# Performance work log

Measured on AMD Instinct MI355X. Metric: run time of the kernel, lower is better.

## Reference

```python
import jax, jax.numpy as jnp
import numpy as np

MAX_DEPTH = 6
NUM_TREES = 64
LEAF_DIMS = 128
D_IN = 512
BATCH = 4096
N_INTERNAL = 2 ** MAX_DEPTH - 1  # 63
N_LEAVES = 2 ** MAX_DEPTH        # 64


def setup_inputs() -> dict:
    key = jax.random.key(0)
    ks = jax.random.split(key, 4)
    x = jax.random.normal(ks[0], (BATCH, D_IN), dtype=jnp.float32)
    # Stacked internal-node dense layers, node i at index i (level order, node_index ordering)
    W = jax.random.normal(ks[1], (N_INTERNAL, D_IN, NUM_TREES), dtype=jnp.float32) / np.sqrt(D_IN)
    b = jnp.zeros((N_INTERNAL, NUM_TREES), dtype=jnp.float32)
    leaf_weight = jax.random.normal(ks[2], (N_LEAVES, LEAF_DIMS, NUM_TREES), dtype=jnp.float32)
    gates = jax.random.normal(ks[3], (N_LEAVES, LEAF_DIMS, NUM_TREES), dtype=jnp.float32)
    return {"x": x, "W": W, "b": b, "leaf_weight": leaf_weight, "gates": gates}


def reference(x, W, b, leaf_weight, gates):
    # All internal-node gating probabilities in one batched matmul:
    # g[b, n, t] = sigmoid(x[b] @ W[n] + b[n])  for every internal node n, tree t
    g = jax.nn.sigmoid(jnp.einsum('bd,ndt->bnt', x, W) + b[None, :, :])  # [B, 63, T]

    B = x.shape[0]
    T = W.shape[-1]
    # Path probability to each leaf, built level by level.
    # Level l has 2^l nodes at internal indices [2^l - 1, 2^(l+1) - 2];
    # interleaving (left=p*g, right=p*(1-g)) matches node_index child ordering.
    p = jnp.ones((B, 1, T), dtype=x.dtype)
    for level in range(MAX_DEPTH):
        start = 2 ** level - 1
        n_lvl = 2 ** level
        gl = g[:, start:start + n_lvl, :]                  # [B, n_lvl, T]
        children = jnp.stack([p * gl, p * (1.0 - gl)], axis=2)  # [B, n_lvl, 2, T]
        p = children.reshape(B, 2 * n_lvl, T)
    # p: [B, n_leaves, T] leaf path probabilities

    # Softmax mixture-of-experts gate over trees, then weighted leaf mixture:
    # out[b, d] = sum_{l, t} p[b, l, t] * leaf_weight[l, d, t] * softmax(gates, -1)[l, d, t]
    w = leaf_weight * jax.nn.softmax(gates, axis=-1)  # [L, D, T]
    out = jnp.einsum('blt,ldt->bd', p, w)
    return out
```

## Files before the change

### kernel.cpp

```cpp
#include <hip/hip_runtime.h>
#include <stdint.h>

#define BATCH 4096
#define DIN   512
#define NT    64
#define NL    64
#define LD    128
#define KTOT  4096

typedef __attribute__((ext_vector_type(8))) short bf16x8;
typedef __attribute__((ext_vector_type(4))) float f32x4;

typedef const __attribute__((address_space(1))) unsigned char* gcp_t;
typedef __attribute__((address_space(3))) unsigned char* lp_t;

__device__ __forceinline__ void gl_lds16(const void* g, void* l) {
  __builtin_amdgcn_global_load_lds((gcp_t)g, (lp_t)l, 16, 0, 0);
}

__device__ __forceinline__ unsigned short f2bf(float f) {
  union { float f; unsigned u; } a; a.f = f;
  unsigned r = a.u + 0x7FFFu + ((a.u >> 16) & 1u);
  return (unsigned short)(r >> 16);
}

__global__ void prep_x_k(const float* __restrict__ x, unsigned short* __restrict__ xb) {
  int i = blockIdx.x * 256 + threadIdx.x;
  float4 v = ((const float4*)x)[i];
  ushort4 o;
  o.x = f2bf(v.x); o.y = f2bf(v.y); o.z = f2bf(v.z); o.w = f2bf(v.w);
  ((ushort4*)xb)[i] = o;
}

__global__ void prep_wt_k(const float* __restrict__ W, unsigned short* __restrict__ Wt) {
  __shared__ float buf[128 * 64];
  int n = blockIdx.x;
  int tid = threadIdx.x;
  for (int d0 = 0; d0 < 512; d0 += 128) {
    if (n < 63) {
      for (int it = 0; it < 32; ++it) {
        int idx = it * 256 + tid;
        buf[idx] = W[n * 32768 + (d0 + (idx >> 6)) * 64 + (idx & 63)];
      }
    }
    __syncthreads();
    int t = tid >> 2, q = tid & 3;
    unsigned short vals[32];
    #pragma unroll
    for (int j = 0; j < 32; ++j)
      vals[j] = (n < 63) ? f2bf(buf[(q * 32 + j) * 64 + t]) : (unsigned short)0;
    uint4* dst = (uint4*)(Wt + t * 32768 + n * 512 + d0 + q * 32);
    const uint4* src = (const uint4*)vals;
    dst[0] = src[0]; dst[1] = src[1]; dst[2] = src[2]; dst[3] = src[3];
    __syncthreads();
  }
}

__global__ void prep_wv_k(const float* __restrict__ gates, const float* __restrict__ lw,
                          unsigned short* __restrict__ Wv2) {
  __shared__ float gb[4096];
  __shared__ float lb[4096];
  __shared__ float wv[4096];
  int d = blockIdx.x;
  int tid = threadIdx.x;
  for (int it = 0; it < 16; ++it) {
    int idx = it * 256 + tid;
    int l = idx >> 6, t = idx & 63;
    int ga = l * 8192 + d * 64 + t;
    gb[idx] = gates[ga];
    lb[idx] = lw[ga];
  }
  __syncthreads();
  int wave = tid >> 6, lane = tid & 63;
  for (int l = wave; l < 64; l += 4) {
    float v = gb[l * 64 + lane];
    float mx = v;
    for (int m = 32; m >= 1; m >>= 1) mx = fmaxf(mx, __shfl_xor(mx, m));
    float e = __expf(v - mx);
    float s = e;
    for (int m = 32; m >= 1; m >>= 1) s += __shfl_xor(s, m);
    wv[l * 64 + lane] = lb[l * 64 + lane] * e / s;
  }
  __syncthreads();
  #pragma unroll
  for (int c = 0; c < 2; ++c) {
    int k0 = tid * 16 + c * 8;
    union { unsigned short u[8]; uint4 v; } o;
    #pragma unroll
    for (int j = 0; j < 8; ++j) {
      int k = k0 + j;
      o.u[j] = f2bf(wv[(k & 63) * 64 + (k >> 6)]);
    }
    *(uint4*)(Wv2 + (long)d * 4096 + k0) = o.v;
  }
}

__global__ __launch_bounds__(256, 2) void gemm1_tree_k(
    const unsigned short* __restrict__ xb,
    const unsigned short* __restrict__ Wt,
    const float* __restrict__ bias,
    unsigned short* __restrict__ P)
{
  __shared__ unsigned short As[128 * 32];
  __shared__ unsigned short Bs[128 * 32];
  __shared__ _Float16 gbuf[128 * 128];
  __shared__ float bb[128];

  const int tid = threadIdx.x;
  const int wave = tid >> 6, lane = tid & 63;
  const int b0 = blockIdx.x * 128;
  const int t0 = blockIdx.y * 2;

  if (tid < 128) {
    int n = tid & 63, t = t0 + (tid >> 6);
    bb[tid] = (n < 63) ? bias[n * 64 + t] : 0.0f;
  }

  const f32x4 zero = {0.f, 0.f, 0.f, 0.f};
  f32x4 acc[4][4];
  #pragma unroll
  for (int i = 0; i < 4; ++i)
    #pragma unroll
    for (int j = 0; j < 4; ++j) acc[i][j] = zero;

  const int g0 = wave * 64 + lane;
  const int g1 = g0 + 256;
  const unsigned short* Ag0 = xb + (long)(b0 + (g0 >> 2)) * 512 + (g0 & 3) * 8;
  const unsigned short* Ag1 = xb + (long)(b0 + (g1 >> 2)) * 512 + (g1 & 3) * 8;
  const unsigned short* Bg0 = Wt + (long)(t0 * 64 + (g0 >> 2)) * 512 + (g0 & 3) * 8;
  const unsigned short* Bg1 = Wt + (long)(t0 * 64 + (g1 >> 2)) * 512 + (g1 & 3) * 8;
  unsigned short* lA0 = As + (wave * 64) * 8;
  unsigned short* lA1 = As + (wave * 64 + 256) * 8;
  unsigned short* lB0 = Bs + (wave * 64) * 8;
  unsigned short* lB1 = Bs + (wave * 64 + 256) * 8;

  const int wm = (wave >> 1) * 64, wn = (wave & 1) * 64;
  const int mrow = lane & 15, kg = lane >> 4;

  for (int kk = 0; kk < 512; kk += 32) {
    __syncthreads();
    gl_lds16(Ag0 + kk, lA0);
    gl_lds16(Ag1 + kk, lA1);
    gl_lds16(Bg0 + kk, lB0);
    gl_lds16(Bg1 + kk, lB1);
    asm volatile("s_waitcnt vmcnt(0)" ::: "memory");
    __syncthreads();

    bf16x8 fa[4], fb[4];
    #pragma unroll
    for (int i = 0; i < 4; ++i)
      fa[i] = *(const bf16x8*)(As + (wm + i * 16 + mrow) * 32 + kg * 8);
    #pragma unroll
    for (int j = 0; j < 4; ++j)
      fb[j] = *(const bf16x8*)(Bs + (wn + j * 16 + mrow) * 32 + kg * 8);
    #pragma unroll
    for (int i = 0; i < 4; ++i)
      #pragma unroll
      for (int j = 0; j < 4; ++j)
        acc[i][j] = __builtin_amdgcn_mfma_f32_16x16x32_bf16(fa[i], fb[j], acc[i][j], 0, 0, 0);
  }

  #pragma unroll
  for (int i = 0; i < 4; ++i)
    #pragma unroll
    for (int j = 0; j < 4; ++j) {
      int col = wn + j * 16 + mrow;
      float bv = bb[col];
      #pragma unroll
      for (int r = 0; r < 4; ++r) {
        int row = wm + i * 16 + kg * 4 + r;
        float z = acc[i][j][r] + bv;
        gbuf[row * 128 + col] = (_Float16)(1.0f / (1.0f + __expf(-z)));
      }
    }
  __syncthreads();

  #pragma unroll
  for (int cc = 0; cc < 8; ++cc) {
    int chunk = cc * 256 + tid;
    int row = chunk >> 4;
    int tr  = (chunk >> 3) & 1;
    int oct = chunk & 7;
    const _Float16* grow = gbuf + row * 128 + tr * 64;
    int l0 = oct * 8;
    float pre = 1.0f;
    #pragma unroll
    for (int lev = 0; lev < 3; ++lev) {
      int node = (1 << lev) - 1 + (l0 >> (6 - lev));
      float g = (float)grow[node];
      pre *= ((l0 >> (5 - lev)) & 1) ? (1.0f - g) : g;
    }
    union { unsigned short u[8]; uint4 v; } ou;
    #pragma unroll
    for (int j = 0; j < 8; ++j) {
      int l = l0 + j;
      float p = pre;
      #pragma unroll
      for (int lev = 3; lev < 6; ++lev) {
        int node = (1 << lev) - 1 + (l >> (6 - lev));
        float g = (float)grow[node];
        p *= ((l >> (5 - lev)) & 1) ? (1.0f - g) : g;
      }
      ou.u[j] = f2bf(p);
    }
    *(uint4*)(P + (long)(b0 + row) * 4096 + (t0 + tr) * 64 + l0) = ou.v;
  }
}

__global__ __launch_bounds__(256, 2) void gemm2_k(
    const unsigned short* __restrict__ P,
    const unsigned short* __restrict__ Wv2,
    float* __restrict__ part)
{
  __shared__ unsigned short As[128 * 32];
  __shared__ unsigned short Bs[128 * 32];
  const int tid = threadIdx.x;
  const int wave = tid >> 6, lane = tid & 63;
  const int b0 = blockIdx.x * 128;
  const int kc = blockIdx.y;

  const f32x4 zero = {0.f, 0.f, 0.f, 0.f};
  f32x4 acc[4][4];
  #pragma unroll
  for (int i = 0; i < 4; ++i)
    #pragma unroll
    for (int j = 0; j < 4; ++j) acc[i][j] = zero;

  const int g0 = wave * 64 + lane;
  const int g1 = g0 + 256;
  const unsigned short* Ag0 = P + (long)(b0 + (g0 >> 2)) * 4096 + kc * 512 + (g0 & 3) * 8;
  const unsigned short* Ag1 = P + (long)(b0 + (g1 >> 2)) * 4096 + kc * 512 + (g1 & 3) * 8;
  const unsigned short* Bg0 = Wv2 + (long)(g0 >> 2) * 4096 + kc * 512 + (g0 & 3) * 8;
  const unsigned short* Bg1 = Wv2 + (long)(g1 >> 2) * 4096 + kc * 512 + (g1 & 3) * 8;
  unsigned short* lA0 = As + (wave * 64) * 8;
  unsigned short* lA1 = As + (wave * 64 + 256) * 8;
  unsigned short* lB0 = Bs + (wave * 64) * 8;
  unsigned short* lB1 = Bs + (wave * 64 + 256) * 8;

  const int wm = (wave >> 1) * 64, wn = (wave & 1) * 64;
  const int mrow = lane & 15, kg = lane >> 4;

  for (int kk = 0; kk < 512; kk += 32) {
    __syncthreads();
    gl_lds16(Ag0 + kk, lA0);
    gl_lds16(Ag1 + kk, lA1);
    gl_lds16(Bg0 + kk, lB0);
    gl_lds16(Bg1 + kk, lB1);
    asm volatile("s_waitcnt vmcnt(0)" ::: "memory");
    __syncthreads();

    bf16x8 fa[4], fb[4];
    #pragma unroll
    for (int i = 0; i < 4; ++i)
      fa[i] = *(const bf16x8*)(As + (wm + i * 16 + mrow) * 32 + kg * 8);
    #pragma unroll
    for (int j = 0; j < 4; ++j)
      fb[j] = *(const bf16x8*)(Bs + (wn + j * 16 + mrow) * 32 + kg * 8);
    #pragma unroll
    for (int i = 0; i < 4; ++i)
      #pragma unroll
      for (int j = 0; j < 4; ++j)
        acc[i][j] = __builtin_amdgcn_mfma_f32_16x16x32_bf16(fa[i], fb[j], acc[i][j], 0, 0, 0);
  }

  float* dst = part + (long)kc * (4096 * 128);
  #pragma unroll
  for (int i = 0; i < 4; ++i)
    #pragma unroll
    for (int j = 0; j < 4; ++j) {
      int col = wn + j * 16 + mrow;
      #pragma unroll
      for (int r = 0; r < 4; ++r) {
        int row = wm + i * 16 + kg * 4 + r;
        dst[(long)(b0 + row) * 128 + col] = acc[i][j][r];
      }
    }
}

__global__ void reduce8_k(const float* __restrict__ part, float* __restrict__ out) {
  int i = blockIdx.x * 256 + threadIdx.x;
  float4 s = ((const float4*)part)[i];
  #pragma unroll
  for (int k = 1; k < 8; ++k) {
    float4 v = ((const float4*)part)[k * 131072 + i];
    s.x += v.x; s.y += v.y; s.z += v.z; s.w += v.w;
  }
  ((float4*)out)[i] = s;
}

extern "C" void kernel_launch(void* const* d_in, const int* in_sizes, int n_in,
                              void* d_out, int out_size, void* d_ws, size_t ws_size,
                              hipStream_t stream) {
  const float* x     = (const float*)d_in[0];
  const float* W     = (const float*)d_in[1];
  const float* b     = (const float*)d_in[2];
  const float* lw    = (const float*)d_in[3];
  const float* gates = (const float*)d_in[4];
  float* out = (float*)d_out;

  char* ws = (char*)d_ws;
  unsigned short* xb  = (unsigned short*)(ws);
  unsigned short* Wt  = (unsigned short*)(ws + (4l  << 20));
  unsigned short* Wv2 = (unsigned short*)(ws + (8l  << 20));
  unsigned short* P   = (unsigned short*)(ws + (16l << 20));
  float*          prt = (float*)(ws + (48l << 20));

  hipLaunchKernelGGL(prep_x_k,     dim3(2048),   dim3(256), 0, stream, x, xb);
  hipLaunchKernelGGL(prep_wt_k,    dim3(64),     dim3(256), 0, stream, W, Wt);
  hipLaunchKernelGGL(prep_wv_k,    dim3(128),    dim3(256), 0, stream, gates, lw, Wv2);
  hipLaunchKernelGGL(gemm1_tree_k, dim3(32, 32), dim3(256), 0, stream, xb, Wt, b, P);
  hipLaunchKernelGGL(gemm2_k,      dim3(32, 8),  dim3(256), 0, stream, P, Wv2, prt);
  hipLaunchKernelGGL(reduce8_k,    dim3(512),    dim3(256), 0, stream, prt, out);
}
```

Measured before the change: 158.8 us.

## Fuse prep kernels, split W transpose finer, replace split-K reduce with atomics

Merges the three preprocessing kernels into one launch and splits the W transpose into 256 blocks instead of 64, which gives that stage more parallelism. It drops the split-K partial buffer and the reduce kernel: gemm2 now atomically adds into the output, which is zeroed by a memset first. It also raises the gemm1 occupancy hint from 2 to 3 blocks per CU. This removes launches and the 16 MB partial write and read, in exchange for atomic traffic, nondeterministic summation order, and possible register spills in gemm1.

```diff
diff --git a/kernel.cpp b/kernel.cpp
--- a/kernel.cpp
+++ b/kernel.cpp
@@ -6,7 +6,6 @@
 #define NT    64
 #define NL    64
 #define LD    128
-#define KTOT  4096
 
 typedef __attribute__((ext_vector_type(8))) short bf16x8;
 typedef __attribute__((ext_vector_type(4))) float f32x4;
@@ -24,19 +23,25 @@
   return (unsigned short)(r >> 16);
 }
 
-__global__ void prep_x_k(const float* __restrict__ x, unsigned short* __restrict__ xb) {
-  int i = blockIdx.x * 256 + threadIdx.x;
-  float4 v = ((const float4*)x)[i];
-  ushort4 o;
-  o.x = f2bf(v.x); o.y = f2bf(v.y); o.z = f2bf(v.z); o.w = f2bf(v.w);
-  ((ushort4*)xb)[i] = o;
-}
-
-__global__ void prep_wt_k(const float* __restrict__ W, unsigned short* __restrict__ Wt) {
-  __shared__ float buf[128 * 64];
-  int n = blockIdx.x;
-  int tid = threadIdx.x;
-  for (int d0 = 0; d0 < 512; d0 += 128) {
+__global__ __launch_bounds__(256) void prep_all_k(
+    const float* __restrict__ x, const float* __restrict__ W,
+    const float* __restrict__ gates, const float* __restrict__ lw,
+    unsigned short* __restrict__ xb, unsigned short* __restrict__ Wt,
+    unsigned short* __restrict__ Wv2) {
+  __shared__ float smem[12288];
+  const int bx = blockIdx.x;
+  const int tid = threadIdx.x;
+
+  if (bx < 2048) {
+    int i = bx * 256 + tid;
+    float4 v = ((const float4*)x)[i];
+    ushort4 o;
+    o.x = f2bf(v.x); o.y = f2bf(v.y); o.z = f2bf(v.z); o.w = f2bf(v.w);
+    ((ushort4*)xb)[i] = o;
+  } else if (bx < 2304) {
+    int bb = bx - 2048;
+    int n = bb >> 2, d0 = (bb & 3) * 128;
+    float* buf = smem;
     if (n < 63) {
       for (int it = 0; it < 32; ++it) {
         int idx = it * 256 + tid;
@@ -52,50 +57,45 @@
     uint4* dst = (uint4*)(Wt + t * 32768 + n * 512 + d0 + q * 32);
     const uint4* src = (const uint4*)vals;
     dst[0] = src[0]; dst[1] = src[1]; dst[2] = src[2]; dst[3] = src[3];
-    __syncthreads();
-  }
-}
-
-__global__ void prep_wv_k(const float* __restrict__ gates, const float* __restrict__ lw,
-                          unsigned short* __restrict__ Wv2) {
-  __shared__ float gb[4096];
-  __shared__ float lb[4096];
-  __shared__ float wv[4096];
-  int d = blockIdx.x;
-  int tid = threadIdx.x;
-  for (int it = 0; it < 16; ++it) {
-    int idx = it * 256 + tid;
-    int l = idx >> 6, t = idx & 63;
-    int ga = l * 8192 + d * 64 + t;
-    gb[idx] = gates[ga];
-    lb[idx] = lw[ga];
-  }
-  __syncthreads();
-  int wave = tid >> 6, lane = tid & 63;
-  for (int l = wave; l < 64; l += 4) {
-    float v = gb[l * 64 + lane];
-    float mx = v;
-    for (int m = 32; m >= 1; m >>= 1) mx = fmaxf(mx, __shfl_xor(mx, m));
-    float e = __expf(v - mx);
-    float s = e;
-    for (int m = 32; m >= 1; m >>= 1) s += __shfl_xor(s, m);
-    wv[l * 64 + lane] = lb[l * 64 + lane] * e / s;
-  }
-  __syncthreads();
-  #pragma unroll
-  for (int c = 0; c < 2; ++c) {
-    int k0 = tid * 16 + c * 8;
-    union { unsigned short u[8]; uint4 v; } o;
-    #pragma unroll
-    for (int j = 0; j < 8; ++j) {
-      int k = k0 + j;
-      o.u[j] = f2bf(wv[(k & 63) * 64 + (k >> 6)]);
-    }
-    *(uint4*)(Wv2 + (long)d * 4096 + k0) = o.v;
-  }
-}
-
-__global__ __launch_bounds__(256, 2) void gemm1_tree_k(
+  } else {
+    int d = bx - 2304;
+    float* gb = smem;
+    float* lb = smem + 4096;
+    float* wv = smem + 8192;
+    for (int it = 0; it < 16; ++it) {
+      int idx = it * 256 + tid;
+      int l = idx >> 6;
+      int ga = l * 8192 + d * 64 + (idx & 63);
+      gb[idx] = gates[ga];
+      lb[idx] = lw[ga];
+    }
+    __syncthreads();
+    int wave = tid >> 6, lane = tid & 63;
+    for (int l = wave; l < 64; l += 4) {
+      float v = gb[l * 64 + lane];
+      float mx = v;
+      for (int m = 32; m >= 1; m >>= 1) mx = fmaxf(mx, __shfl_xor(mx, m));
+      float e = __expf(v - mx);
+      float s = e;
+      for (int m = 32; m >= 1; m >>= 1) s += __shfl_xor(s, m);
+      wv[l * 64 + lane] = lb[l * 64 + lane] * e / s;
+    }
+    __syncthreads();
+    #pragma unroll
+    for (int c = 0; c < 2; ++c) {
+      int k0 = tid * 16 + c * 8;
+      union { unsigned short u[8]; uint4 v; } o;
+      #pragma unroll
+      for (int j = 0; j < 8; ++j) {
+        int k = k0 + j;
+        o.u[j] = f2bf(wv[(k & 63) * 64 + (k >> 6)]);
+      }
+      *(uint4*)(Wv2 + (long)d * 4096 + k0) = o.v;
+    }
+  }
+}
+
+__global__ __launch_bounds__(256, 3) void gemm1_tree_k(
     const unsigned short* __restrict__ xb,
     const unsigned short* __restrict__ Wt,
     const float* __restrict__ bias,
@@ -210,7 +210,7 @@
 __global__ __launch_bounds__(256, 2) void gemm2_k(
     const unsigned short* __restrict__ P,
     const unsigned short* __restrict__ Wv2,
-    float* __restrict__ part)
+    float* __restrict__ out)
 {
   __shared__ unsigned short As[128 * 32];
   __shared__ unsigned short Bs[128 * 32];
@@ -263,7 +263,6 @@
         acc[i][j] = __builtin_amdgcn_mfma_f32_16x16x32_bf16(fa[i], fb[j], acc[i][j], 0, 0, 0);
   }
 
-  float* dst = part + (long)kc * (4096 * 128);
   #pragma unroll
   for (int i = 0; i < 4; ++i)
     #pragma unroll
@@ -272,20 +271,9 @@
       #pragma unroll
       for (int r = 0; r < 4; ++r) {
         int row = wm + i * 16 + kg * 4 + r;
-        dst[(long)(b0 + row) * 128 + col] = acc[i][j][r];
-      }
-    }
-}
-
-__global__ void reduce8_k(const float* __restrict__ part, float* __restrict__ out) {
-  int i = blockIdx.x * 256 + threadIdx.x;
-  float4 s = ((const float4*)part)[i];
-  #pragma unroll
-  for (int k = 1; k < 8; ++k) {
-    float4 v = ((const float4*)part)[k * 131072 + i];
-    s.x += v.x; s.y += v.y; s.z += v.z; s.w += v.w;
-  }
-  ((float4*)out)[i] = s;
+        atomicAdd(&out[(long)(b0 + row) * 128 + col], acc[i][j][r]);
+      }
+    }
 }
 
 extern "C" void kernel_launch(void* const* d_in, const int* in_sizes, int n_in,
@@ -303,12 +291,10 @@
   unsigned short* Wt  = (unsigned short*)(ws + (4l  << 20));
   unsigned short* Wv2 = (unsigned short*)(ws + (8l  << 20));
   unsigned short* P   = (unsigned short*)(ws + (16l << 20));
-  float*          prt = (float*)(ws + (48l << 20));
-
-  hipLaunchKernelGGL(prep_x_k,     dim3(2048),   dim3(256), 0, stream, x, xb);
-  hipLaunchKernelGGL(prep_wt_k,    dim3(64),     dim3(256), 0, stream, W, Wt);
-  hipLaunchKernelGGL(prep_wv_k,    dim3(128),    dim3(256), 0, stream, gates, lw, Wv2);
+
+  hipMemsetAsync(out, 0, (size_t)4096 * 128 * sizeof(float), stream);
+  hipLaunchKernelGGL(prep_all_k,   dim3(2432),   dim3(256), 0, stream,
+                     x, W, gates, lw, xb, Wt, Wv2);
   hipLaunchKernelGGL(gemm1_tree_k, dim3(32, 32), dim3(256), 0, stream, xb, Wt, b, P);
-  hipLaunchKernelGGL(gemm2_k,      dim3(32, 8),  dim3(256), 0, stream, P, Wv2, prt);
-  hipLaunchKernelGGL(reduce8_k,    dim3(512),    dim3(256), 0, stream, prt, out);
-}
+  hipLaunchKernelGGL(gemm2_k,      dim3(32, 8),  dim3(256), 0, stream, P, Wv2, out);
+}
```

New measurement: 148.5 us. 1.07x faster.
